# Kernel tuning notes

Measured on AMD Instinct MI355X. Metric: run time of the kernel, lower is better.

The kernel has to match this reference:

```python
import jax, jax.numpy as jnp
import numpy as np
import math

B, S, D = 4, 4096, 2048
HEAD_DIM = 128  # dim_model // head_nums = 2048 // 16
DEPTH = 12


def setup_inputs() -> dict:
    key = jax.random.key(0)
    ks = jax.random.split(key, 8)
    std = 0.1
    return {
        "x": jax.random.normal(ks[0], (B, S, D), dtype=jnp.float32),
        "WQ": jax.random.normal(ks[1], (D, 2 * HEAD_DIM), dtype=jnp.float32) * (D ** -0.5),
        "WK": jax.random.normal(ks[2], (D, 2 * HEAD_DIM), dtype=jnp.float32) * (D ** -0.5),
        "WV": jax.random.normal(ks[3], (D, 2 * HEAD_DIM), dtype=jnp.float32) * (D ** -0.5),
        "lambda_q1": jax.random.normal(ks[4], (HEAD_DIM,), dtype=jnp.float32) * std,
        "lambda_q2": jax.random.normal(ks[5], (HEAD_DIM,), dtype=jnp.float32) * std,
        "lambda_k1": jax.random.normal(ks[6], (HEAD_DIM,), dtype=jnp.float32) * std,
        "lambda_k2": jax.random.normal(ks[7], (HEAD_DIM,), dtype=jnp.float32) * std,
    }


def reference(x, WQ, WK, WV, lambda_q1, lambda_q2, lambda_k1, lambda_k2):
    scale = HEAD_DIM ** -0.5
    lambda_init = 0.8 - 0.6 * math.exp(-0.3 * DEPTH)

    q = x @ WQ                      # [B, S, 2*hd]
    k = x @ WK
    v = x @ WV                      # [B, S, 2*hd]
    q1, q2 = q[..., :HEAD_DIM], q[..., HEAD_DIM:]
    k1, k2 = k[..., :HEAD_DIM], k[..., HEAD_DIM:]

    a1 = jnp.einsum("bqd,bkd->bqk", q1, k1) * scale  # [B, S, S]
    a2 = jnp.einsum("bqd,bkd->bqk", q2, k2) * scale

    lambda_1 = jnp.exp(jnp.sum(lambda_q1 * lambda_k1))
    lambda_2 = jnp.exp(jnp.sum(lambda_q2 * lambda_k2))
    lam = lambda_1 + lambda_2 + lambda_init

    attn = jax.nn.softmax(a1, axis=-1) - lam * jax.nn.softmax(a2, axis=-1)
    return jnp.einsum("bqk,bkd->bqd", attn, v)  # [B, S, 2*hd]
```

## Files before the change

### kernel.cpp

```cpp
#include <hip/hip_runtime.h>
#include <stdint.h>

typedef unsigned short u16;
typedef __attribute__((ext_vector_type(4))) float f32x4;
typedef __attribute__((ext_vector_type(8))) short s16x8;
typedef __attribute__((ext_vector_type(8))) __bf16 bf16x8;
typedef __attribute__((ext_vector_type(8))) unsigned short u16x8;

__device__ __forceinline__ f32x4 mfma16(s16x8 a, s16x8 b, f32x4 c) {
  return __builtin_amdgcn_mfma_f32_16x16x32_bf16(
      __builtin_bit_cast(bf16x8, a), __builtin_bit_cast(bf16x8, b), c, 0, 0, 0);
}

__device__ __forceinline__ void gl_lds16(const u16* g, u16* l) {
  __builtin_amdgcn_global_load_lds(
      (const __attribute__((address_space(1))) void*)g,
      (__attribute__((address_space(3))) void*)l, 16, 0, 0);
}

__device__ __forceinline__ u16 bf16rne(float f) {
  uint32_t u = __builtin_bit_cast(uint32_t, f);
  u += 0x7fffu + ((u >> 16) & 1u);
  return (u16)(u >> 16);
}

__global__ void cast_x_kernel(const float* __restrict__ x, u16* __restrict__ xb) {
  size_t i = ((size_t)blockIdx.x * 256 + threadIdx.x) * 8;
  f32x4 a = *(const f32x4*)(x + i);
  f32x4 b = *(const f32x4*)(x + i + 4);
  u16x8 o;
#pragma unroll
  for (int j = 0; j < 4; ++j) { o[j] = bf16rne(a[j]); o[4 + j] = bf16rne(b[j]); }
  *(u16x8*)(xb + i) = o;
}

__global__ void cast_w_kernel(const float* __restrict__ WQ, const float* __restrict__ WK,
                              const float* __restrict__ WV, u16* __restrict__ Wt, float qscale) {
  int i = blockIdx.x * 256 + threadIdx.x;
  int r = i >> 11, k = i & 2047;
  int sel = r >> 8, c = r & 255;
  const float* W = (sel == 0) ? WQ : (sel == 1) ? WK : WV;
  float v = W[(size_t)k * 256 + c];
  if (sel == 0) v *= qscale;
  Wt[i] = bf16rne(v);
}

__global__ __launch_bounds__(256) void proj_gemm(const u16* __restrict__ xb, const u16* __restrict__ Wt,
                                                 u16* __restrict__ Qb, u16* __restrict__ Kb,
                                                 u16* __restrict__ Vb) {
  const int m0 = blockIdx.x * 128, n0 = blockIdx.y * 128;
  const int tid = threadIdx.x, lane = tid & 63, w = tid >> 6;
  const int ln = lane & 15, quad = lane >> 4;
  const int wm = w & 1, wn = w >> 1;
  __shared__ __align__(16) u16 As[128 * 32];
  __shared__ __align__(16) u16 Bs[128 * 32];
  f32x4 acc[4][4];
#pragma unroll
  for (int i = 0; i < 4; ++i)
#pragma unroll
    for (int j = 0; j < 4; ++j) acc[i][j] = f32x4{0.f, 0.f, 0.f, 0.f};

  for (int kk = 0; kk < 2048; kk += 32) {
    __syncthreads();
#pragma unroll
    for (int i = 0; i < 2; ++i) {
      int p = tid + i * 256;
      int row = p >> 2, cg = (p & 3) ^ (row & 3);
      gl_lds16(xb + (size_t)(m0 + row) * 2048 + kk + cg * 8, As + (size_t)(p - lane) * 8);
      gl_lds16(Wt + (size_t)(n0 + row) * 2048 + kk + cg * 8, Bs + (size_t)(p - lane) * 8);
    }
    __syncthreads();
    s16x8 a[4];
#pragma unroll
    for (int mt = 0; mt < 4; ++mt) {
      int r = wm * 64 + mt * 16 + ln;
      a[mt] = *(const s16x8*)(As + r * 32 + ((quad ^ (r & 3)) * 8));
    }
#pragma unroll
    for (int nt = 0; nt < 4; ++nt) {
      int r = wn * 64 + nt * 16 + ln;
      s16x8 bf = *(const s16x8*)(Bs + r * 32 + ((quad ^ (r & 3)) * 8));
#pragma unroll
      for (int mt = 0; mt < 4; ++mt) acc[mt][nt] = mfma16(a[mt], bf, acc[mt][nt]);
    }
  }
#pragma unroll
  for (int mt = 0; mt < 4; ++mt)
#pragma unroll
    for (int nt = 0; nt < 4; ++nt)
#pragma unroll
      for (int j = 0; j < 4; ++j) {
        int row = m0 + wm * 64 + mt * 16 + quad * 4 + j;
        int col = n0 + wn * 64 + nt * 16 + ln;
        u16 v = bf16rne(acc[mt][nt][j]);
        int sel = col >> 8, c = col & 255;
        u16* dst = (sel == 0) ? Qb : (sel == 1) ? Kb : Vb;
        dst[(size_t)row * 256 + c] = v;
      }
}

__global__ void transpose_v(const u16* __restrict__ Vb, u16* __restrict__ Vt) {
  const int s0 = blockIdx.x * 64, c0 = blockIdx.y * 64, b = blockIdx.z;
  const int tid = threadIdx.x;
  __shared__ u16 T[64][72];
#pragma unroll
  for (int it = 0; it < 2; ++it) {
    int idx = tid + it * 256;
    int r = idx >> 3, vc = idx & 7;
    *(u16x8*)(&T[r][vc * 8]) =
        *(const u16x8*)(Vb + ((size_t)(b * 4096 + s0 + r)) * 256 + c0 + vc * 8);
  }
  __syncthreads();
#pragma unroll
  for (int it = 0; it < 2; ++it) {
    int idx = tid + it * 256;
    int cr = idx >> 3, sv = idx & 7;
    u16x8 v;
#pragma unroll
    for (int j = 0; j < 8; ++j) v[j] = T[sv * 8 + j][cr];
    *(u16x8*)(Vt + ((size_t)(b * 256 + c0 + cr)) * 4096 + s0 + sv * 8) = v;
  }
}

__global__ void lam_kernel(const float* __restrict__ lq1, const float* __restrict__ lq2,
                           const float* __restrict__ lk1, const float* __restrict__ lk2,
                           float* __restrict__ lamp) {
  int t = threadIdx.x;
  float d1 = lq1[t] * lk1[t] + lq1[t + 64] * lk1[t + 64];
  float d2 = lq2[t] * lk2[t] + lq2[t + 64] * lk2[t + 64];
#pragma unroll
  for (int off = 32; off; off >>= 1) {
    d1 += __shfl_xor(d1, off);
    d2 += __shfl_xor(d2, off);
  }
  if (t == 0) *lamp = expf(d1) + expf(d2) + (0.8f - 0.6f * expf(-3.6f));
}

__global__ __launch_bounds__(256, 3) void attn_kernel(const u16* __restrict__ Qb,
                                                      const u16* __restrict__ Kb,
                                                      const u16* __restrict__ Vt,
                                                      float* __restrict__ Op,
                                                      float* __restrict__ lp) {
  const int qt = blockIdx.x, mh = blockIdx.y, b = blockIdx.z;
  const int map = mh >> 1, half = mh & 1;
  const int tid = threadIdx.x, lane = tid & 63, w = tid >> 6;
  const int ln = lane & 15, quad = lane >> 4;

  __shared__ __align__(16) u16 Ks[64 * 128];
  __shared__ __align__(16) u16 Vs[256 * 64];
  u16* Ps = Ks;

  s16x8 aq[4];
  {
    int qrow = qt * 64 + w * 16 + ln;
    const u16* qp = Qb + ((size_t)(b * 4096 + qrow)) * 256 + map * 128 + quad * 8;
#pragma unroll
    for (int kt = 0; kt < 4; ++kt) aq[kt] = *(const s16x8*)(qp + kt * 32);
  }

  f32x4 o[4][4];
#pragma unroll
  for (int mt = 0; mt < 4; ++mt)
#pragma unroll
    for (int nt = 0; nt < 4; ++nt) o[mt][nt] = f32x4{0.f, 0.f, 0.f, 0.f};
  float l_run[4] = {0.f, 0.f, 0.f, 0.f};

  const u16* Kg0 = Kb + ((size_t)b * 4096) * 256 + map * 128;
  const u16* Vg0 = Vt + (size_t)b * 256 * 4096;
  const int kb0 = half * 2048;

  for (int kb = kb0; kb < kb0 + 2048; kb += 64) {
    __syncthreads();
#pragma unroll
    for (int i = 0; i < 4; ++i) {
      int p = tid + i * 256;
      int row = p >> 4, cg = (p & 15) ^ (row & 15);
      gl_lds16(Kg0 + (size_t)(kb + row) * 256 + cg * 8, Ks + (size_t)(p - lane) * 8);
    }
#pragma unroll
    for (int i = 0; i < 8; ++i) {
      int p = tid + i * 256;
      int row = p >> 3, cg = (p & 7) ^ (row & 7);
      gl_lds16(Vg0 + (size_t)row * 4096 + kb + cg * 8, Vs + (size_t)(p - lane) * 8);
    }
    __syncthreads();

    f32x4 s[4];
#pragma unroll
    for (int nt = 0; nt < 4; ++nt) s[nt] = f32x4{0.f, 0.f, 0.f, 0.f};
#pragma unroll
    for (int kt = 0; kt < 4; ++kt)
#pragma unroll
      for (int nt = 0; nt < 4; ++nt) {
        int r = nt * 16 + ln;
        int cp = (kt * 4 + quad) ^ (r & 15);
        s16x8 bk = *(const s16x8*)(Ks + r * 128 + cp * 8);
        s[nt] = mfma16(aq[kt], bk, s[nt]);
      }

#pragma unroll
    for (int nt = 0; nt < 4; ++nt)
#pragma unroll
      for (int j = 0; j < 4; ++j) {
        float pv = exp2f(s[nt][j]);
        s[nt][j] = pv;
        l_run[j] += pv;
      }

    __syncthreads();
#pragma unroll
    for (int nt = 0; nt < 4; ++nt)
#pragma unroll
      for (int j = 0; j < 4; ++j)
        Ps[(w * 16 + quad * 4 + j) * 72 + nt * 16 + ln] = bf16rne(s[nt][j]);
    __syncthreads();

    s16x8 ap[4][2];
#pragma unroll
    for (int mt = 0; mt < 4; ++mt)
#pragma unroll
      for (int k2 = 0; k2 < 2; ++k2)
        ap[mt][k2] = *(const s16x8*)(Ps + (mt * 16 + ln) * 72 + k2 * 32 + quad * 8);

#pragma unroll
    for (int nt = 0; nt < 4; ++nt)
#pragma unroll
      for (int k2 = 0; k2 < 2; ++k2) {
        int vc = w * 64 + nt * 16 + ln;
        int cp = (k2 * 4 + quad) ^ (vc & 7);
        s16x8 bv = *(const s16x8*)(Vs + vc * 64 + cp * 8);
#pragma unroll
        for (int mt = 0; mt < 4; ++mt) o[mt][nt] = mfma16(ap[mt][k2], bv, o[mt][nt]);
      }
  }

#pragma unroll
  for (int off = 8; off; off >>= 1)
#pragma unroll
    for (int j = 0; j < 4; ++j) l_run[j] += __shfl_xor(l_run[j], off);

  float* Og = Op + (size_t)mh * 16384 * 256 + (size_t)b * 4096 * 256;
  float* lg = lp + (size_t)mh * 16384 + (size_t)b * 4096;
  if (ln == 0) {
#pragma unroll
    for (int j = 0; j < 4; ++j) lg[qt * 64 + w * 16 + quad * 4 + j] = l_run[j];
  }
#pragma unroll
  for (int mt = 0; mt < 4; ++mt)
#pragma unroll
    for (int nt = 0; nt < 4; ++nt)
#pragma unroll
      for (int j = 0; j < 4; ++j) {
        size_t row = (size_t)(qt * 64 + mt * 16 + quad * 4 + j);
        Og[row * 256 + w * 64 + nt * 16 + ln] = o[mt][nt][j];
      }
}

__global__ void combine_kernel(const float* __restrict__ Op, const float* __restrict__ lp,
                               const float* __restrict__ lamp, float* __restrict__ out) {
  size_t i = ((size_t)blockIdx.x * 256 + threadIdx.x) * 4;
  size_t row = i >> 8;
  const size_t MS = (size_t)16384 * 256;
  float lam = *lamp;
  float r1 = 1.f / (lp[row] + lp[16384 + row]);
  float r2 = 1.f / (lp[2 * 16384 + row] + lp[3 * 16384 + row]);
  f32x4 a0 = *(const f32x4*)(Op + i);
  f32x4 a1 = *(const f32x4*)(Op + MS + i);
  f32x4 b0 = *(const f32x4*)(Op + 2 * MS + i);
  f32x4 b1 = *(const f32x4*)(Op + 3 * MS + i);
  f32x4 r;
#pragma unroll
  for (int j = 0; j < 4; ++j) r[j] = (a0[j] + a1[j]) * r1 - lam * (b0[j] + b1[j]) * r2;
  *(f32x4*)(out + i) = r;
}

extern "C" void kernel_launch(void* const* d_in, const int* in_sizes, int n_in,
                              void* d_out, int out_size, void* d_ws, size_t ws_size,
                              hipStream_t stream) {
  (void)in_sizes; (void)n_in; (void)out_size; (void)ws_size;
  const float* x   = (const float*)d_in[0];
  const float* WQ  = (const float*)d_in[1];
  const float* WK  = (const float*)d_in[2];
  const float* WV  = (const float*)d_in[3];
  const float* lq1 = (const float*)d_in[4];
  const float* lq2 = (const float*)d_in[5];
  const float* lk1 = (const float*)d_in[6];
  const float* lk2 = (const float*)d_in[7];
  float* out = (float*)d_out;

  char* ws = (char*)d_ws;
  u16* xb = (u16*)ws;   ws += (size_t)16384 * 2048 * 2;
  u16* Wt = (u16*)ws;   ws += (size_t)768 * 2048 * 2;
  u16* Qb = (u16*)ws;   ws += (size_t)16384 * 256 * 2;
  u16* Kb = (u16*)ws;   ws += (size_t)16384 * 256 * 2;
  u16* Vb = (u16*)ws;   ws += (size_t)16384 * 256 * 2;
  u16* Vt = (u16*)ws;   ws += (size_t)16384 * 256 * 2;
  float* Op = (float*)ws; ws += (size_t)4 * 16384 * 256 * 4;
  float* lp = (float*)ws; ws += (size_t)4 * 16384 * 4;
  float* lamp = (float*)ws;

  const float qscale = 0.0883883476f * 1.44269504f;

  hipLaunchKernelGGL(cast_x_kernel, dim3(16384), dim3(256), 0, stream, x, xb);
  hipLaunchKernelGGL(cast_w_kernel, dim3(6144), dim3(256), 0, stream, WQ, WK, WV, Wt, qscale);
  hipLaunchKernelGGL(proj_gemm, dim3(128, 6), dim3(256), 0, stream, xb, Wt, Qb, Kb, Vb);
  hipLaunchKernelGGL(transpose_v, dim3(64, 4, 4), dim3(256), 0, stream, Vb, Vt);
  hipLaunchKernelGGL(lam_kernel, dim3(1), dim3(64), 0, stream, lq1, lq2, lk1, lk2, lamp);
  hipLaunchKernelGGL(attn_kernel, dim3(64, 4, 4), dim3(256), 0, stream, Qb, Kb, Vt, Op, lp);
  hipLaunchKernelGGL(combine_kernel, dim3(4096), dim3(256), 0, stream, Op, lp, lamp, out);
}
```

Measured before the change: 465.8 us.

## Fuse V transpose into projection, share V tile across both maps with 32x32 MFMA

Result: no change. 475.0 us (+2.0%).

```diff
diff --git a/kernel.cpp b/kernel.cpp
--- a/kernel.cpp
+++ b/kernel.cpp
@@ -3,12 +3,18 @@
 
 typedef unsigned short u16;
 typedef __attribute__((ext_vector_type(4))) float f32x4;
+typedef __attribute__((ext_vector_type(16))) float f32x16;
 typedef __attribute__((ext_vector_type(8))) short s16x8;
 typedef __attribute__((ext_vector_type(8))) __bf16 bf16x8;
 typedef __attribute__((ext_vector_type(8))) unsigned short u16x8;
+typedef __attribute__((ext_vector_type(4))) unsigned short u16x4;
 
 __device__ __forceinline__ f32x4 mfma16(s16x8 a, s16x8 b, f32x4 c) {
   return __builtin_amdgcn_mfma_f32_16x16x32_bf16(
+      __builtin_bit_cast(bf16x8, a), __builtin_bit_cast(bf16x8, b), c, 0, 0, 0);
+}
+__device__ __forceinline__ f32x16 mfma32(s16x8 a, s16x8 b, f32x16 c) {
+  return __builtin_amdgcn_mfma_f32_32x32x16_bf16(
       __builtin_bit_cast(bf16x8, a), __builtin_bit_cast(bf16x8, b), c, 0, 0, 0);
 }
 
@@ -47,8 +53,11 @@
 
 __global__ __launch_bounds__(256) void proj_gemm(const u16* __restrict__ xb, const u16* __restrict__ Wt,
                                                  u16* __restrict__ Qb, u16* __restrict__ Kb,
-                                                 u16* __restrict__ Vb) {
-  const int m0 = blockIdx.x * 128, n0 = blockIdx.y * 128;
+                                                 u16* __restrict__ Vt) {
+  const int bid = blockIdx.x;
+  const int xcd = bid & 7, j = bid >> 3;
+  const int m0 = (xcd * 16 + (j / 6)) * 128;
+  const int n0 = (j % 6) * 128;
   const int tid = threadIdx.x, lane = tid & 63, w = tid >> 6;
   const int ln = lane & 15, quad = lane >> 4;
   const int wm = w & 1, wn = w >> 1;
@@ -58,7 +67,7 @@
 #pragma unroll
   for (int i = 0; i < 4; ++i)
 #pragma unroll
-    for (int j = 0; j < 4; ++j) acc[i][j] = f32x4{0.f, 0.f, 0.f, 0.f};
+    for (int jj = 0; jj < 4; ++jj) acc[i][jj] = f32x4{0.f, 0.f, 0.f, 0.f};
 
   for (int kk = 0; kk < 2048; kk += 32) {
     __syncthreads();
@@ -87,39 +96,22 @@
 #pragma unroll
   for (int mt = 0; mt < 4; ++mt)
 #pragma unroll
-    for (int nt = 0; nt < 4; ++nt)
-#pragma unroll
-      for (int j = 0; j < 4; ++j) {
-        int row = m0 + wm * 64 + mt * 16 + quad * 4 + j;
-        int col = n0 + wn * 64 + nt * 16 + ln;
-        u16 v = bf16rne(acc[mt][nt][j]);
-        int sel = col >> 8, c = col & 255;
-        u16* dst = (sel == 0) ? Qb : (sel == 1) ? Kb : Vb;
-        dst[(size_t)row * 256 + c] = v;
+    for (int nt = 0; nt < 4; ++nt) {
+      int row0 = m0 + wm * 64 + mt * 16 + quad * 4;
+      int col = n0 + wn * 64 + nt * 16 + ln;
+      int sel = col >> 8, c = col & 255;
+      u16x4 vv;
+#pragma unroll
+      for (int jj = 0; jj < 4; ++jj) vv[jj] = bf16rne(acc[mt][nt][jj]);
+      if (sel == 2) {
+        int b = row0 >> 12, s = row0 & 4095;
+        *(u16x4*)(Vt + (size_t)b * 1048576 + (size_t)c * 4096 + s) = vv;
+      } else {
+        u16* dst = (sel == 0) ? Qb : Kb;
+#pragma unroll
+        for (int jj = 0; jj < 4; ++jj) dst[(size_t)(row0 + jj) * 256 + c] = vv[jj];
       }
-}
-
-__global__ void transpose_v(const u16* __restrict__ Vb, u16* __restrict__ Vt) {
-  const int s0 = blockIdx.x * 64, c0 = blockIdx.y * 64, b = blockIdx.z;
-  const int tid = threadIdx.x;
-  __shared__ u16 T[64][72];
-#pragma unroll
-  for (int it = 0; it < 2; ++it) {
-    int idx = tid + it * 256;
-    int r = idx >> 3, vc = idx & 7;
-    *(u16x8*)(&T[r][vc * 8]) =
-        *(const u16x8*)(Vb + ((size_t)(b * 4096 + s0 + r)) * 256 + c0 + vc * 8);
-  }
-  __syncthreads();
-#pragma unroll
-  for (int it = 0; it < 2; ++it) {
-    int idx = tid + it * 256;
-    int cr = idx >> 3, sv = idx & 7;
-    u16x8 v;
-#pragma unroll
-    for (int j = 0; j < 8; ++j) v[j] = T[sv * 8 + j][cr];
-    *(u16x8*)(Vt + ((size_t)(b * 256 + c0 + cr)) * 4096 + s0 + sv * 8) = v;
-  }
+    }
 }
 
 __global__ void lam_kernel(const float* __restrict__ lq1, const float* __restrict__ lq2,
@@ -136,123 +128,129 @@
   if (t == 0) *lamp = expf(d1) + expf(d2) + (0.8f - 0.6f * expf(-3.6f));
 }
 
-__global__ __launch_bounds__(256, 3) void attn_kernel(const u16* __restrict__ Qb,
+__global__ __launch_bounds__(256, 2) void attn_kernel(const u16* __restrict__ Qb,
                                                       const u16* __restrict__ Kb,
                                                       const u16* __restrict__ Vt,
                                                       float* __restrict__ Op,
                                                       float* __restrict__ lp) {
-  const int qt = blockIdx.x, mh = blockIdx.y, b = blockIdx.z;
-  const int map = mh >> 1, half = mh & 1;
+  const int qt = blockIdx.x, half = blockIdx.y, b = blockIdx.z;
   const int tid = threadIdx.x, lane = tid & 63, w = tid >> 6;
-  const int ln = lane & 15, quad = lane >> 4;
-
-  __shared__ __align__(16) u16 Ks[64 * 128];
+  const int l5 = lane & 31, lh = lane >> 5;
+  const int mapsel = w & 1, rt = w >> 1;
+
+  __shared__ __align__(16) u16 Ks[64 * 256];
   __shared__ __align__(16) u16 Vs[256 * 64];
   u16* Ps = Ks;
 
-  s16x8 aq[4];
+  s16x8 aq[8];
   {
-    int qrow = qt * 64 + w * 16 + ln;
-    const u16* qp = Qb + ((size_t)(b * 4096 + qrow)) * 256 + map * 128 + quad * 8;
-#pragma unroll
-    for (int kt = 0; kt < 4; ++kt) aq[kt] = *(const s16x8*)(qp + kt * 32);
-  }
-
-  f32x4 o[4][4];
-#pragma unroll
-  for (int mt = 0; mt < 4; ++mt)
-#pragma unroll
-    for (int nt = 0; nt < 4; ++nt) o[mt][nt] = f32x4{0.f, 0.f, 0.f, 0.f};
-  float l_run[4] = {0.f, 0.f, 0.f, 0.f};
-
-  const u16* Kg0 = Kb + ((size_t)b * 4096) * 256 + map * 128;
-  const u16* Vg0 = Vt + (size_t)b * 256 * 4096;
+    const u16* qp = Qb + ((size_t)(b * 4096 + qt * 64 + rt * 32 + l5)) * 256 +
+                    mapsel * 128 + lh * 8;
+#pragma unroll
+    for (int st = 0; st < 8; ++st) aq[st] = *(const s16x8*)(qp + st * 16);
+  }
+
+  f32x16 O[2][4];
+#pragma unroll
+  for (int i = 0; i < 2; ++i)
+#pragma unroll
+    for (int jj = 0; jj < 4; ++jj)
+#pragma unroll
+      for (int r = 0; r < 16; ++r) O[i][jj][r] = 0.f;
+  float l_run[16];
+#pragma unroll
+  for (int r = 0; r < 16; ++r) l_run[r] = 0.f;
+
+  const u16* Kg0 = Kb + ((size_t)b * 4096) * 256;
+  const u16* Vg0 = Vt + (size_t)b * 1048576;
   const int kb0 = half * 2048;
 
   for (int kb = kb0; kb < kb0 + 2048; kb += 64) {
     __syncthreads();
-#pragma unroll
-    for (int i = 0; i < 4; ++i) {
-      int p = tid + i * 256;
-      int row = p >> 4, cg = (p & 15) ^ (row & 15);
-      gl_lds16(Kg0 + (size_t)(kb + row) * 256 + cg * 8, Ks + (size_t)(p - lane) * 8);
-    }
 #pragma unroll
     for (int i = 0; i < 8; ++i) {
       int p = tid + i * 256;
-      int row = p >> 3, cg = (p & 7) ^ (row & 7);
+      int row = p >> 5, c = p & 31;
+      int cg = (c & 16) | ((c ^ row) & 15);
+      gl_lds16(Kg0 + (size_t)(kb + row) * 256 + cg * 8, Ks + (size_t)(p - lane) * 8);
+    }
+#pragma unroll
+    for (int i = 0; i < 8; ++i) {
+      int p = tid + i * 256;
+      int row = p >> 3, c = p & 7;
+      int cg = c ^ (row & 7);
       gl_lds16(Vg0 + (size_t)row * 4096 + kb + cg * 8, Vs + (size_t)(p - lane) * 8);
     }
     __syncthreads();
 
-    f32x4 s[4];
-#pragma unroll
-    for (int nt = 0; nt < 4; ++nt) s[nt] = f32x4{0.f, 0.f, 0.f, 0.f};
-#pragma unroll
-    for (int kt = 0; kt < 4; ++kt)
-#pragma unroll
-      for (int nt = 0; nt < 4; ++nt) {
-        int r = nt * 16 + ln;
-        int cp = (kt * 4 + quad) ^ (r & 15);
-        s16x8 bk = *(const s16x8*)(Ks + r * 128 + cp * 8);
-        s[nt] = mfma16(aq[kt], bk, s[nt]);
+    f32x16 S0, S1;
+#pragma unroll
+    for (int r = 0; r < 16; ++r) { S0[r] = 0.f; S1[r] = 0.f; }
+#pragma unroll
+    for (int st = 0; st < 8; ++st) {
+      int c = mapsel * 16 + st * 2 + lh;
+      int ph0 = (c & 16) | ((c ^ l5) & 15);
+      s16x8 b0 = *(const s16x8*)(Ks + l5 * 256 + ph0 * 8);
+      s16x8 b1 = *(const s16x8*)(Ks + (32 + l5) * 256 + ph0 * 8);
+      S0 = mfma32(aq[st], b0, S0);
+      S1 = mfma32(aq[st], b1, S1);
+    }
+
+    __syncthreads();
+    {
+      int qbase = mapsel * 64 + rt * 32 + 4 * lh;
+#pragma unroll
+      for (int r = 0; r < 16; ++r) {
+        float p0 = exp2f(S0[r]);
+        float p1 = exp2f(S1[r]);
+        l_run[r] += p0 + p1;
+        int qrow = qbase + (r & 3) + 8 * (r >> 2);
+        Ps[qrow * 72 + l5] = bf16rne(p0);
+        Ps[qrow * 72 + 32 + l5] = bf16rne(p1);
       }
-
-#pragma unroll
-    for (int nt = 0; nt < 4; ++nt)
-#pragma unroll
-      for (int j = 0; j < 4; ++j) {
-        float pv = exp2f(s[nt][j]);
-        s[nt][j] = pv;
-        l_run[j] += pv;
+    }
+    __syncthreads();
+
+#pragma unroll
+    for (int ks = 0; ks < 4; ++ks) {
+      s16x8 ap0 = *(const s16x8*)(Ps + (mapsel * 64 + l5) * 72 + ks * 16 + lh * 8);
+      s16x8 ap1 = *(const s16x8*)(Ps + (mapsel * 64 + 32 + l5) * 72 + ks * 16 + lh * 8);
+      int c = ks * 2 + lh;
+#pragma unroll
+      for (int ct = 0; ct < 4; ++ct) {
+        int n = (w >> 1) * 128 + ct * 32 + l5;
+        s16x8 bv = *(const s16x8*)(Vs + n * 64 + ((c ^ (n & 7)) * 8));
+        O[0][ct] = mfma32(ap0, bv, O[0][ct]);
+        O[1][ct] = mfma32(ap1, bv, O[1][ct]);
       }
-
-    __syncthreads();
-#pragma unroll
-    for (int nt = 0; nt < 4; ++nt)
-#pragma unroll
-      for (int j = 0; j < 4; ++j)
-        Ps[(w * 16 + quad * 4 + j) * 72 + nt * 16 + ln] = bf16rne(s[nt][j]);
-    __syncthreads();
-
-    s16x8 ap[4][2];
-#pragma unroll
-    for (int mt = 0; mt < 4; ++mt)
-#pragma unroll
-      for (int k2 = 0; k2 < 2; ++k2)
-        ap[mt][k2] = *(const s16x8*)(Ps + (mt * 16 + ln) * 72 + k2 * 32 + quad * 8);
-
-#pragma unroll
-    for (int nt = 0; nt < 4; ++nt)
-#pragma unroll
-      for (int k2 = 0; k2 < 2; ++k2) {
-        int vc = w * 64 + nt * 16 + ln;
-        int cp = (k2 * 4 + quad) ^ (vc & 7);
-        s16x8 bv = *(const s16x8*)(Vs + vc * 64 + cp * 8);
-#pragma unroll
-        for (int mt = 0; mt < 4; ++mt) o[mt][nt] = mfma16(ap[mt][k2], bv, o[mt][nt]);
-      }
-  }
-
-#pragma unroll
-  for (int off = 8; off; off >>= 1)
-#pragma unroll
-    for (int j = 0; j < 4; ++j) l_run[j] += __shfl_xor(l_run[j], off);
-
-  float* Og = Op + (size_t)mh * 16384 * 256 + (size_t)b * 4096 * 256;
+    }
+  }
+
+#pragma unroll
+  for (int off = 16; off; off >>= 1)
+#pragma unroll
+    for (int r = 0; r < 16; ++r) l_run[r] += __shfl_xor(l_run[r], off);
+
+  const int mh = mapsel * 2 + half;
+  const size_t MS = (size_t)16384 * 256;
+  float* Og = Op + (size_t)mh * MS + (size_t)b * 4096 * 256;
   float* lg = lp + (size_t)mh * 16384 + (size_t)b * 4096;
-  if (ln == 0) {
-#pragma unroll
-    for (int j = 0; j < 4; ++j) lg[qt * 64 + w * 16 + quad * 4 + j] = l_run[j];
-  }
-#pragma unroll
-  for (int mt = 0; mt < 4; ++mt)
-#pragma unroll
-    for (int nt = 0; nt < 4; ++nt)
-#pragma unroll
-      for (int j = 0; j < 4; ++j) {
-        size_t row = (size_t)(qt * 64 + mt * 16 + quad * 4 + j);
-        Og[row * 256 + w * 64 + nt * 16 + ln] = o[mt][nt][j];
+  if (l5 == 0) {
+#pragma unroll
+    for (int r = 0; r < 16; ++r) {
+      int qg = qt * 64 + rt * 32 + 4 * lh + (r & 3) + 8 * (r >> 2);
+      lg[qg] = l_run[r];
+    }
+  }
+#pragma unroll
+  for (int rt2 = 0; rt2 < 2; ++rt2)
+#pragma unroll
+    for (int ct = 0; ct < 4; ++ct)
+#pragma unroll
+      for (int r = 0; r < 16; ++r) {
+        int qg = qt * 64 + rt2 * 32 + (r & 3) + 8 * (r >> 2) + 4 * lh;
+        int col = (w >> 1) * 128 + ct * 32 + l5;
+        Og[(size_t)qg * 256 + col] = O[rt2][ct][r];
       }
 }
 
@@ -293,7 +291,6 @@
   u16* Wt = (u16*)ws;   ws += (size_t)768 * 2048 * 2;
   u16* Qb = (u16*)ws;   ws += (size_t)16384 * 256 * 2;
   u16* Kb = (u16*)ws;   ws += (size_t)16384 * 256 * 2;
-  u16* Vb = (u16*)ws;   ws += (size_t)16384 * 256 * 2;
   u16* Vt = (u16*)ws;   ws += (size_t)16384 * 256 * 2;
   float* Op = (float*)ws; ws += (size_t)4 * 16384 * 256 * 4;
   float* lp = (float*)ws; ws += (size_t)4 * 16384 * 4;
@@ -303,9 +300,8 @@
 
   hipLaunchKernelGGL(cast_x_kernel, dim3(16384), dim3(256), 0, stream, x, xb);
   hipLaunchKernelGGL(cast_w_kernel, dim3(6144), dim3(256), 0, stream, WQ, WK, WV, Wt, qscale);
-  hipLaunchKernelGGL(proj_gemm, dim3(128, 6), dim3(256), 0, stream, xb, Wt, Qb, Kb, Vb);
-  hipLaunchKernelGGL(transpose_v, dim3(64, 4, 4), dim3(256), 0, stream, Vb, Vt);
+  hipLaunchKernelGGL(proj_gemm, dim3(768), dim3(256), 0, stream, xb, Wt, Qb, Kb, Vt);
   hipLaunchKernelGGL(lam_kernel, dim3(1), dim3(64), 0, stream, lq1, lq2, lk1, lk2, lamp);
-  hipLaunchKernelGGL(attn_kernel, dim3(64, 4, 4), dim3(256), 0, stream, Qb, Kb, Vt, Op, lp);
+  hipLaunchKernelGGL(attn_kernel, dim3(64, 2, 4), dim3(256), 0, stream, Qb, Kb, Vt, Op, lp);
   hipLaunchKernelGGL(combine_kernel, dim3(4096), dim3(256), 0, stream, Op, lp, lamp, out);
 }
```
